# Kernel optimization log

Measured on AMD Instinct MI355X. Metric: run time of the kernel, lower is better.

The kernel has to match this reference:

```python
import jax, jax.numpy as jnp
import numpy as np

NUM_HEADS = 16

def setup_inputs() -> dict:
    key = jax.random.key(0)
    ks = jax.random.split(key, 5)
    B, L, H = 4, 1024, 1024
    s = 0.02
    return {
        'x': jax.random.normal(ks[0], (B, L, H), jnp.float32),
        'Wq': jax.random.normal(ks[1], (H, H), jnp.float32) * s,
        'Wkv_short': jax.random.normal(ks[2], (H, 2 * H), jnp.float32) * s,
        'Wkv_long': jax.random.normal(ks[3], (H, 2 * H), jnp.float32) * s,
        'Wo': jax.random.normal(ks[4], (H, H), jnp.float32) * s,
        'mix_weight': jnp.float32(0.5),
        'decay_factor': jnp.float32(0.95),
    }

def _heads(t, B, L, nh, hd):
    # [B, L, H] -> [B, nh, L, hd]
    return t.reshape(B, L, nh, hd).transpose(0, 2, 1, 3)

def _attention(q, k, v, bias):
    # q,k,v: [B, nh, L, hd]; bias: [L, L] or None
    hd = q.shape[-1]
    scores = jnp.einsum('bhqd,bhkd->bhqk', q, k) / jnp.sqrt(jnp.float32(hd))
    if bias is not None:
        scores = scores + bias[None, None]
    attn = jax.nn.softmax(scores, axis=-1)
    return jnp.einsum('bhqk,bhkd->bhqd', attn, v)

def reference(x, Wq, Wkv_short, Wkv_long, Wo, mix_weight, decay_factor):
    B, L, H = x.shape
    nh = NUM_HEADS
    hd = H // nh
    q = _heads(x @ Wq, B, L, nh, hd)
    kv_s = x @ Wkv_short
    k_s = _heads(kv_s[..., :H], B, L, nh, hd)
    v_s = _heads(kv_s[..., H:], B, L, nh, hd)
    pos = jnp.arange(L, dtype=jnp.float32)
    decay_bias = -jnp.abs(pos[None, :] - pos[:, None]) * (1.0 - decay_factor)
    out_short = _attention(q, k_s, v_s, decay_bias)
    kv_l = x @ Wkv_long
    k_l = _heads(kv_l[..., :H], B, L, nh, hd)
    v_l = _heads(kv_l[..., H:], B, L, nh, hd)
    out_long = _attention(q, k_l, v_l, None)
    alpha = jax.nn.sigmoid(mix_weight)
    out = alpha * out_short + (1.0 - alpha) * out_long
    out = out.transpose(0, 2, 1, 3).reshape(B, L, H)
    return out @ Wo
```

## Files before the change

### kernel.cpp

```cpp
#include <hip/hip_runtime.h>
#include <hip/hip_bf16.h>
#include <math.h>
#include <stdint.h>

typedef unsigned short u16;
typedef __attribute__((ext_vector_type(8))) short bf16x8;
typedef __attribute__((ext_vector_type(4))) float f32x4;
typedef __attribute__((ext_vector_type(4))) unsigned short u16x4;
typedef __attribute__((ext_vector_type(4))) unsigned int uint32x4;

#define MFMA_BF16(A, B, C) __builtin_amdgcn_mfma_f32_16x16x32_bf16((A), (B), (C), 0, 0, 0)

__device__ __forceinline__ void async16(const void* g, const void* l) {
    __builtin_amdgcn_global_load_lds(
        (const __attribute__((address_space(1))) unsigned int*)(uintptr_t)g,
        (__attribute__((address_space(3))) unsigned int*)(uintptr_t)l, 16, 0, 0);
}

__device__ __forceinline__ u16 f2bf(float f) {
    unsigned u = __float_as_uint(f);
    u += 0x7fffu + ((u >> 16) & 1u);
    return (u16)(u >> 16);
}

__device__ __forceinline__ unsigned pack2(float a, float b) {
    __hip_bfloat162 h = __float22bfloat162_rn(float2{a, b});
    return *reinterpret_cast<unsigned*>(&h);
}

__device__ __forceinline__ float bf2f(u16 v) {
    unsigned u = ((unsigned)v) << 16;
    return __uint_as_float(u);
}

__device__ __forceinline__ bf16x8 mk_frag(unsigned w0, unsigned w1,
                                          unsigned w2, unsigned w3) {
    uint32x4 u = {w0, w1, w2, w3};
    return __builtin_bit_cast(bf16x8, u);
}

__global__ __launch_bounds__(256) void cvt_x(const float* __restrict__ x,
                                             u16* __restrict__ xb) {
    int i = blockIdx.x * 256 + threadIdx.x;
    float4 v = ((const float4*)x)[i];
    u16x4 o = {f2bf(v.x), f2bf(v.y), f2bf(v.z), f2bf(v.w)};
    ((u16x4*)xb)[i] = o;
}

__global__ __launch_bounds__(256) void cvt_w_all(
    const float* __restrict__ Wq, const float* __restrict__ Wks,
    const float* __restrict__ Wkl, const float* __restrict__ Wo,
    u16* __restrict__ wqt, u16* __restrict__ wkst,
    u16* __restrict__ wklt, u16* __restrict__ wot)
{
    __shared__ float tile[32][33];
    int x = blockIdx.x;
    const float* W; u16* Wt; int N, nb;
    if (x < 32)       { W = Wq;  Wt = wqt;  N = 1024; nb = x * 32; }
    else if (x < 96)  { W = Wks; Wt = wkst; N = 2048; nb = (x - 32) * 32; }
    else if (x < 160) { W = Wkl; Wt = wklt; N = 2048; nb = (x - 96) * 32; }
    else              { W = Wo;  Wt = wot;  N = 1024; nb = (x - 160) * 32; }
    int kb = blockIdx.y * 32;
    int t = threadIdx.x;
    int r = t >> 3, c4 = (t & 7) * 4;
    float4 v = *(const float4*)&W[(size_t)(kb + r) * N + nb + c4];
    tile[r][c4] = v.x; tile[r][c4 + 1] = v.y;
    tile[r][c4 + 2] = v.z; tile[r][c4 + 3] = v.w;
    __syncthreads();
    u16x4 o = {f2bf(tile[c4 + 0][r]), f2bf(tile[c4 + 1][r]),
               f2bf(tile[c4 + 2][r]), f2bf(tile[c4 + 3][r])};
    *(u16x4*)&Wt[(size_t)(nb + r) * 1024 + kb + c4] = o;
}

__global__ __launch_bounds__(256) void gemm_proj(
    const u16* __restrict__ A, const u16* __restrict__ wq,
    const u16* __restrict__ wks, const u16* __restrict__ wkl,
    u16* __restrict__ qd, u16* __restrict__ ksd, u16* __restrict__ vsd,
    u16* __restrict__ kld, u16* __restrict__ vld)
{
    __shared__ u16 Alds[128][32];
    __shared__ u16 Blds[128][32];
    const int cx = blockIdx.x;
    const u16* Bt; u16* dK; u16* dV; int colBase; float osc = 1.0f;
    bool ktype;
    if (cx < 8)       { Bt = wq;  colBase = cx * 128;        dK = qd;  dV = nullptr;
                        osc = 0.18033688f; ktype = true; }
    else if (cx < 24) { Bt = wks; colBase = (cx - 8) * 128;  dK = ksd; dV = vsd;
                        ktype = (cx < 16); }
    else              { Bt = wkl; colBase = (cx - 24) * 128; dK = kld; dV = vld;
                        ktype = (cx < 32); }

    const int t = threadIdx.x;
    const int l = t & 63, w = t >> 6;
    const int wm = w & 1, wn = w >> 1;
    const int rowBase = blockIdx.y * 128;
    const int lc = l & 15, lr4 = l >> 4;

    f32x4 acc[4][4];
#pragma unroll
    for (int i = 0; i < 4; i++)
#pragma unroll
        for (int j = 0; j < 4; j++) acc[i][j] = (f32x4){0.f, 0.f, 0.f, 0.f};

    const int srow = w * 32 + (l >> 2);
    const int sc8  = (((l & 3) ^ ((l >> 2) & 3)) * 8);
    const u16* Ag = A  + (size_t)(rowBase + srow) * 1024 + sc8;
    const u16* Bg = Bt + (size_t)(colBase + srow) * 1024 + sc8;
    const int sw = (lc & 3);

    const u16 (*Lm)[32] = ktype ? Blds : Alds;
    const u16 (*Ln)[32] = ktype ? Alds : Blds;

    for (int kt = 0; kt < 32; ++kt) {
        __syncthreads();
        const int ko = kt * 32;
        async16(Ag + ko,         &Alds[w * 32][0]);
        async16(Ag + ko + 16384, &Alds[w * 32 + 16][0]);
        async16(Bg + ko,         &Blds[w * 32][0]);
        async16(Bg + ko + 16384, &Blds[w * 32 + 16][0]);
        __syncthreads();

        bf16x8 af[4], bf[4];
#pragma unroll
        for (int mt = 0; mt < 4; ++mt)
            af[mt] = *(const bf16x8*)&Lm[wm * 64 + mt * 16 + lc][(lr4 ^ sw) * 8];
#pragma unroll
        for (int nt = 0; nt < 4; ++nt)
            bf[nt] = *(const bf16x8*)&Ln[wn * 64 + nt * 16 + lc][(lr4 ^ sw) * 8];
#pragma unroll
        for (int mt = 0; mt < 4; ++mt)
#pragma unroll
            for (int nt = 0; nt < 4; ++nt)
                acc[mt][nt] = MFMA_BF16(af[mt], bf[nt], acc[mt][nt]);
    }

    if (ktype) {
#pragma unroll
        for (int mt = 0; mt < 4; ++mt)
#pragma unroll
            for (int nt = 0; nt < 4; ++nt) {
                int f   = colBase + wm * 64 + mt * 16 + lr4 * 4;
                int tok = rowBase + wn * 64 + nt * 16 + lc;
                int b = tok >> 10, tk = tok & 1023;
                int head = (f >> 6) & 15, d = f & 63;
                u16x4 pv = {f2bf(acc[mt][nt][0] * osc), f2bf(acc[mt][nt][1] * osc),
                            f2bf(acc[mt][nt][2] * osc), f2bf(acc[mt][nt][3] * osc)};
                *(u16x4*)&dK[((size_t)(b * 16 + head) * 1024 + tk) * 64 + d] = pv;
            }
    } else {
#pragma unroll
        for (int mt = 0; mt < 4; ++mt)
#pragma unroll
            for (int nt = 0; nt < 4; ++nt) {
                int gr0 = rowBase + wm * 64 + mt * 16 + lr4 * 4;
                int gc0 = colBase + wn * 64 + nt * 16;
                int head = gc0 >> 6;
                int b = gr0 >> 10, tok = gr0 & 1023;
                int tokp = (tok & ~31) | (((tok >> 2) & 3) << 3) |
                           (((tok >> 4) & 1) << 2);
                int d = (gc0 & 63) + lc;
                u16x4 pv = {f2bf(acc[mt][nt][0]), f2bf(acc[mt][nt][1]),
                            f2bf(acc[mt][nt][2]), f2bf(acc[mt][nt][3])};
                *(u16x4*)&dV[((size_t)(b * 16 + head - 16) * 64 + d) * 1024 +
                             tokp] = pv;
            }
    }
}

__global__ __launch_bounds__(256) void gemm_out(
    const u16* __restrict__ Aattn, const u16* __restrict__ Bwot,
    float* __restrict__ dst)
{
    __shared__ u16 Alds[64][32];
    __shared__ u16 Blds[128][32];
    const int t = threadIdx.x;
    const int l = t & 63, w = t >> 6;
    const int wm = w & 1, wn = w >> 1;
    const int rowBase = blockIdx.y * 64;
    const int colBase = blockIdx.x * 128;
    const int lc = l & 15, lr4 = l >> 4;

    f32x4 acc[4][2];
#pragma unroll
    for (int i = 0; i < 4; i++)
#pragma unroll
        for (int j = 0; j < 2; j++) acc[i][j] = (f32x4){0.f, 0.f, 0.f, 0.f};

    const int sl  = l >> 2;
    const int sc8 = (((l & 3) ^ (sl & 3)) * 8);
    const u16* Ag = Aattn + (size_t)(rowBase + w * 16 + sl) * 1024 + sc8;
    const u16* Bg = Bwot  + (size_t)(colBase + w * 32 + sl) * 1024 + sc8;
    const int sw = (lc & 3);

    for (int kt = 0; kt < 32; ++kt) {
        __syncthreads();
        const int ko = kt * 32;
        async16(Ag + ko,         &Alds[w * 16][0]);
        async16(Bg + ko,         &Blds[w * 32][0]);
        async16(Bg + ko + 16384, &Blds[w * 32 + 16][0]);
        __syncthreads();

        bf16x8 af[4], bf[2];
#pragma unroll
        for (int mt = 0; mt < 4; ++mt)
            af[mt] = *(const bf16x8*)&Blds[wm * 64 + mt * 16 + lc][(lr4 ^ sw) * 8];
#pragma unroll
        for (int nt = 0; nt < 2; ++nt)
            bf[nt] = *(const bf16x8*)&Alds[wn * 32 + nt * 16 + lc][(lr4 ^ sw) * 8];
#pragma unroll
        for (int mt = 0; mt < 4; ++mt)
#pragma unroll
            for (int nt = 0; nt < 2; ++nt)
                acc[mt][nt] = MFMA_BF16(af[mt], bf[nt], acc[mt][nt]);
    }

#pragma unroll
    for (int mt = 0; mt < 4; ++mt)
#pragma unroll
        for (int nt = 0; nt < 2; ++nt) {
            int f   = colBase + wm * 64 + mt * 16 + lr4 * 4;
            int tok = rowBase + wn * 32 + nt * 16 + lc;
            float4 v = {acc[mt][nt][0], acc[mt][nt][1],
                        acc[mt][nt][2], acc[mt][nt][3]};
            *(float4*)&dst[(size_t)tok * 1024 + f] = v;
        }
}

__global__ __launch_bounds__(256, 4) void attn_mfma(
    const u16* __restrict__ Q, const u16* __restrict__ Ksb,
    const u16* __restrict__ Vsb, const u16* __restrict__ Klb,
    const u16* __restrict__ Vlb, const float* __restrict__ decayf,
    u16* __restrict__ Os, u16* __restrict__ Ol)
{
    __shared__ __align__(16) u16 Kt[2][2][64][32];
    __shared__ __align__(16) u16 Vt[2][2][64][32];

    const int t = threadIdx.x;
    const int l = t & 63, w = t >> 6;
    const int lc = l & 15, lr4 = l >> 4;
    const int h = blockIdx.x, qt = blockIdx.y;
    const int b = blockIdx.z >> 1, branch = blockIdx.z & 1;
    const size_t bh = (size_t)(b * 16 + h);
    const int qbase = qt * 128;
    const u16* Qg = Q + bh * (1024 * 64);
    const u16* Kg = (branch ? Klb : Ksb) + bh * (1024 * 64);
    const u16* Vg = (branch ? Vlb : Vsb) + bh * (64 * 1024);
    u16* outp = branch ? Ol : Os;

    const int sl = l >> 2;
    const int sc = (((l & 3) ^ ((l >> 3) & 3)) * 8);
    const int swr = (lc >> 1) & 3;

    int ktLo = 0, ktHi = 16;
    if (branch == 0) {
        ktLo = qt * 2 - 7; if (ktLo < 0) ktLo = 0;
        ktHi = qt * 2 + 9; if (ktHi > 16) ktHi = 16;
    }

    bf16x8 aQ[2][2];
#pragma unroll
    for (int qg = 0; qg < 2; ++qg)
#pragma unroll
        for (int kh = 0; kh < 2; ++kh)
            aQ[qg][kh] = *(const bf16x8*)&Qg[
                (size_t)(qbase + w * 32 + qg * 16 + lc) * 64 + kh * 32 + lr4 * 8];

    auto stage = [&](int kt, int buf) {
#pragma unroll
        for (int i = 0; i < 4; i++) {
            int id = w * 4 + i;
            int kh = (id >> 2) & 1, ch = id & 3;
            if (id < 8)
                async16(Kg + (size_t)(kt * 64 + ch * 16 + sl) * 64 + kh * 32 + sc,
                        &Kt[buf][kh][ch * 16][0]);
            else
                async16(Vg + (size_t)(ch * 16 + sl) * 1024 + kt * 64 + kh * 32 + sc,
                        &Vt[buf][kh][ch * 16][0]);
        }
    };

    stage(ktLo, 0);
    __syncthreads();

    const float C2 = (1.0f - decayf[0]) * 1.44269504f;
    const float qf = (float)(qbase + w * 32 + lc);

    f32x4 sumv[2] = {(f32x4){0.f, 0.f, 0.f, 0.f}, (f32x4){0.f, 0.f, 0.f, 0.f}};
    f32x4 o[2][4];
#pragma unroll
    for (int qg = 0; qg < 2; ++qg)
#pragma unroll
        for (int dt = 0; dt < 4; ++dt) o[qg][dt] = (f32x4){0.f, 0.f, 0.f, 0.f};

    for (int kt = ktLo, it = 0; kt < ktHi; ++kt, ++it) {
        const int cur = it & 1;
        if (kt + 1 < ktHi) stage(kt + 1, cur ^ 1);

        bf16x8 ak[4][2];
#pragma unroll
        for (int nt = 0; nt < 4; ++nt) {
            ak[nt][0] = *(const bf16x8*)&Kt[cur][0][nt * 16 + lc][(lr4 ^ swr) * 8];
            ak[nt][1] = *(const bf16x8*)&Kt[cur][1][nt * 16 + lc][(lr4 ^ swr) * 8];
        }

        unsigned pw[2][8];
#pragma unroll
        for (int qg = 0; qg < 2; ++qg) {
            const float d0 = qf + (float)(qg * 16 - kt * 64 - lr4 * 4);
            f32x4 s[4];
#pragma unroll
            for (int nt = 0; nt < 4; ++nt) {
                if (branch == 0) {
                    float dd = d0 - (float)(nt * 16);
                    s[nt] = (f32x4){-fabsf(dd) * C2,
                                    -fabsf(dd - 1.0f) * C2,
                                    -fabsf(dd - 2.0f) * C2,
                                    -fabsf(dd - 3.0f) * C2};
                } else {
                    s[nt] = (f32x4){0.f, 0.f, 0.f, 0.f};
                }
                s[nt] = MFMA_BF16(ak[nt][0], aQ[qg][0], s[nt]);
                s[nt] = MFMA_BF16(ak[nt][1], aQ[qg][1], s[nt]);
            }
#pragma unroll
            for (int nt = 0; nt < 4; ++nt) {
                float p0 = __builtin_amdgcn_exp2f(s[nt][0]);
                float p1 = __builtin_amdgcn_exp2f(s[nt][1]);
                float p2 = __builtin_amdgcn_exp2f(s[nt][2]);
                float p3 = __builtin_amdgcn_exp2f(s[nt][3]);
                sumv[qg][0] += p0; sumv[qg][1] += p1;
                sumv[qg][2] += p2; sumv[qg][3] += p3;
                pw[qg][nt * 2]     = pack2(p0, p1);
                pw[qg][nt * 2 + 1] = pack2(p2, p3);
            }
        }

#pragma unroll
        for (int dt = 0; dt < 4; ++dt) {
            bf16x8 v0 = *(const bf16x8*)&Vt[cur][0][dt * 16 + lc][(lr4 ^ swr) * 8];
            bf16x8 v1 = *(const bf16x8*)&Vt[cur][1][dt * 16 + lc][(lr4 ^ swr) * 8];
#pragma unroll
            for (int qg = 0; qg < 2; ++qg) {
                bf16x8 pb0 = mk_frag(pw[qg][0], pw[qg][1], pw[qg][2], pw[qg][3]);
                bf16x8 pb1 = mk_frag(pw[qg][4], pw[qg][5], pw[qg][6], pw[qg][7]);
                o[qg][dt] = MFMA_BF16(v0, pb0, o[qg][dt]);
                o[qg][dt] = MFMA_BF16(v1, pb1, o[qg][dt]);
            }
        }

        __syncthreads();
    }

#pragma unroll
    for (int qg = 0; qg < 2; ++qg) {
        float s = (sumv[qg][0] + sumv[qg][1]) + (sumv[qg][2] + sumv[qg][3]);
        s += __shfl_xor(s, 16);
        s += __shfl_xor(s, 32);
        float inv = 1.0f / s;
        int qrow = qbase + w * 32 + qg * 16 + lc;
        u16* op = outp + ((size_t)(b * 1024) + qrow) * 1024 + h * 64;
#pragma unroll
        for (int dt = 0; dt < 4; ++dt) {
            uint2 w2 = {pack2(o[qg][dt][0] * inv, o[qg][dt][1] * inv),
                        pack2(o[qg][dt][2] * inv, o[qg][dt][3] * inv)};
            *(uint2*)&op[dt * 16 + lr4 * 4] = w2;
        }
    }
}

__global__ __launch_bounds__(256) void mix_kernel(
    const u16* __restrict__ Os, const u16* __restrict__ Ol,
    const float* __restrict__ mixw, u16* __restrict__ dst)
{
    const float a = 1.0f / (1.0f + __expf(-mixw[0]));
    int i = blockIdx.x * 256 + threadIdx.x;
    uint4 s = ((const uint4*)Os)[i];
    uint4 l = ((const uint4*)Ol)[i];
    unsigned su[4] = {s.x, s.y, s.z, s.w};
    unsigned lu[4] = {l.x, l.y, l.z, l.w};
    unsigned ou[4];
#pragma unroll
    for (int k = 0; k < 4; ++k) {
        float s0 = bf2f((u16)su[k]), s1 = bf2f((u16)(su[k] >> 16));
        float l0 = bf2f((u16)lu[k]), l1 = bf2f((u16)(lu[k] >> 16));
        ou[k] = pack2(l0 + a * (s0 - l0), l1 + a * (s1 - l1));
    }
    ((uint4*)dst)[i] = make_uint4(ou[0], ou[1], ou[2], ou[3]);
}

extern "C" void kernel_launch(void* const* d_in, const int* in_sizes, int n_in,
                              void* d_out, int out_size, void* d_ws, size_t ws_size,
                              hipStream_t stream) {
    const float* x      = (const float*)d_in[0];
    const float* Wq     = (const float*)d_in[1];
    const float* Wkvs   = (const float*)d_in[2];
    const float* Wkvl   = (const float*)d_in[3];
    const float* Wo     = (const float*)d_in[4];
    const float* mixw   = (const float*)d_in[5];
    const float* decayf = (const float*)d_in[6];

    const size_t M1 = 1024 * 1024;
    u16* ws    = (u16*)d_ws;
    u16* xb    = ws;
    u16* wqt   = xb + 4 * M1;
    u16* wkvst = wqt + 1 * M1;
    u16* wkvlt = wkvst + 2 * M1;
    u16* wot   = wkvlt + 2 * M1;
    u16* qb    = wot + 1 * M1;
    u16* ksb   = qb + 4 * M1;
    u16* vsb   = ksb + 4 * M1;
    u16* klb   = vsb + 4 * M1;
    u16* vlb   = klb + 4 * M1;
    u16* attnb = vlb + 4 * M1;
    u16* osb   = xb;
    u16* olb   = wqt;

    cvt_x<<<4096, 256, 0, stream>>>(x, xb);
    cvt_w_all<<<dim3(192, 32), 256, 0, stream>>>(Wq, Wkvs, Wkvl, Wo,
                                                 wqt, wkvst, wkvlt, wot);
    gemm_proj<<<dim3(40, 32), 256, 0, stream>>>(xb, wqt, wkvst, wkvlt,
                                                qb, ksb, vsb, klb, vlb);
    attn_mfma<<<dim3(16, 8, 8), 256, 0, stream>>>(qb, ksb, vsb, klb, vlb,
                                                  decayf, osb, olb);
    mix_kernel<<<2048, 256, 0, stream>>>(osb, olb, mixw, attnb);
    gemm_out<<<dim3(8, 64), 256, 0, stream>>>(attnb, wot, (float*)d_out);
}
```

Baseline: 232.1 us.

## Double-buffer projection GEMM LDS and widen tiles to 128x256

The projection GEMM now uses 128x256 output tiles (a 4x8 MFMA accumulator grid per wave) and double-buffers the async global-to-LDS loads, so the next K slice is fetched while the current one is multiplied. This drops one barrier per iteration and halves the block count, aiming to hide load latency and raise arithmetic intensity. The cost is more registers and LDS per block, which lowers occupancy and parallelism (a 640-block grid, with launch bounds requesting 2 blocks per CU). V-output head indexing is adjusted to the new local column base.

Result: slower. 238.3 us (+2.7%).

```diff
diff --git a/kernel.cpp b/kernel.cpp
--- a/kernel.cpp
+++ b/kernel.cpp
@@ -72,75 +72,97 @@
     *(u16x4*)&Wt[(size_t)(nb + r) * 1024 + kb + c4] = o;
 }
 
-__global__ __launch_bounds__(256) void gemm_proj(
+__global__ __launch_bounds__(256, 2) void gemm_proj(
     const u16* __restrict__ A, const u16* __restrict__ wq,
     const u16* __restrict__ wks, const u16* __restrict__ wkl,
     u16* __restrict__ qd, u16* __restrict__ ksd, u16* __restrict__ vsd,
     u16* __restrict__ kld, u16* __restrict__ vld)
 {
-    __shared__ u16 Alds[128][32];
-    __shared__ u16 Blds[128][32];
+    __shared__ u16 Alds[2][128][32];
+    __shared__ u16 Blds[2][256][32];
     const int cx = blockIdx.x;
-    const u16* Bt; u16* dK; u16* dV; int colBase; float osc = 1.0f;
+    const u16* Bt; u16* dK; u16* dV; int colMat, colLoc; float osc = 1.0f;
     bool ktype;
-    if (cx < 8)       { Bt = wq;  colBase = cx * 128;        dK = qd;  dV = nullptr;
-                        osc = 0.18033688f; ktype = true; }
-    else if (cx < 24) { Bt = wks; colBase = (cx - 8) * 128;  dK = ksd; dV = vsd;
-                        ktype = (cx < 16); }
-    else              { Bt = wkl; colBase = (cx - 24) * 128; dK = kld; dV = vld;
-                        ktype = (cx < 32); }
+    if (cx < 4) {
+        Bt = wq; ktype = true; colLoc = cx * 256; colMat = colLoc;
+        dK = qd; dV = nullptr; osc = 0.18033688f;
+    } else if (cx < 12) {
+        Bt = wks; ktype = (cx < 8);
+        if (ktype) { colLoc = (cx - 4) * 256; colMat = colLoc; }
+        else       { colLoc = (cx - 8) * 256; colMat = 1024 + colLoc; }
+        dK = ksd; dV = vsd;
+    } else {
+        Bt = wkl; ktype = (cx < 16);
+        if (ktype) { colLoc = (cx - 12) * 256; colMat = colLoc; }
+        else       { colLoc = (cx - 16) * 256; colMat = 1024 + colLoc; }
+        dK = kld; dV = vld;
+    }
 
     const int t = threadIdx.x;
     const int l = t & 63, w = t >> 6;
-    const int wm = w & 1, wn = w >> 1;
     const int rowBase = blockIdx.y * 128;
     const int lc = l & 15, lr4 = l >> 4;
 
-    f32x4 acc[4][4];
+    f32x4 acc[4][8];
 #pragma unroll
     for (int i = 0; i < 4; i++)
 #pragma unroll
-        for (int j = 0; j < 4; j++) acc[i][j] = (f32x4){0.f, 0.f, 0.f, 0.f};
-
-    const int srow = w * 32 + (l >> 2);
-    const int sc8  = (((l & 3) ^ ((l >> 2) & 3)) * 8);
-    const u16* Ag = A  + (size_t)(rowBase + srow) * 1024 + sc8;
-    const u16* Bg = Bt + (size_t)(colBase + srow) * 1024 + sc8;
+        for (int j = 0; j < 8; j++) acc[i][j] = (f32x4){0.f, 0.f, 0.f, 0.f};
+
+    const int sl  = l >> 2;
+    const int sc8 = (((l & 3) ^ (sl & 3)) * 8);
+    const u16* Ag = A  + (size_t)(rowBase + w * 32 + sl) * 1024 + sc8;
+    const u16* Bg = Bt + (size_t)(colMat  + w * 64 + sl) * 1024 + sc8;
     const int sw = (lc & 3);
 
-    const u16 (*Lm)[32] = ktype ? Blds : Alds;
-    const u16 (*Ln)[32] = ktype ? Alds : Blds;
+    auto stage = [&](int kt, int buf) {
+        const int ko = kt * 32;
+        async16(Ag + ko,             &Alds[buf][w * 32][0]);
+        async16(Ag + ko + 16 * 1024, &Alds[buf][w * 32 + 16][0]);
+        async16(Bg + ko,             &Blds[buf][w * 64][0]);
+        async16(Bg + ko + 16 * 1024, &Blds[buf][w * 64 + 16][0]);
+        async16(Bg + ko + 32 * 1024, &Blds[buf][w * 64 + 32][0]);
+        async16(Bg + ko + 48 * 1024, &Blds[buf][w * 64 + 48][0]);
+    };
+
+    const int mOff = ktype ? w * 64 : (w & 1) * 64;
+    const int nOff = ktype ? 0      : (w >> 1) * 128;
+
+    stage(0, 0);
+    __syncthreads();
 
     for (int kt = 0; kt < 32; ++kt) {
+        const int cur = kt & 1;
+        if (kt + 1 < 32) stage(kt + 1, cur ^ 1);
+
+        const u16 (*Ab)[32] = Alds[cur];
+        const u16 (*Bb)[32] = Blds[cur];
+        const u16 (*Lm)[32] = ktype ? Bb : Ab;
+        const u16 (*Ln)[32] = ktype ? Ab : Bb;
+
+        bf16x8 af[4], bf[8];
+#pragma unroll
+        for (int mt = 0; mt < 4; ++mt)
+            af[mt] = *(const bf16x8*)&Lm[mOff + mt * 16 + lc][(lr4 ^ sw) * 8];
+#pragma unroll
+        for (int nt = 0; nt < 8; ++nt)
+            bf[nt] = *(const bf16x8*)&Ln[nOff + nt * 16 + lc][(lr4 ^ sw) * 8];
+#pragma unroll
+        for (int mt = 0; mt < 4; ++mt)
+#pragma unroll
+            for (int nt = 0; nt < 8; ++nt)
+                acc[mt][nt] = MFMA_BF16(af[mt], bf[nt], acc[mt][nt]);
+
         __syncthreads();
-        const int ko = kt * 32;
-        async16(Ag + ko,         &Alds[w * 32][0]);
-        async16(Ag + ko + 16384, &Alds[w * 32 + 16][0]);
-        async16(Bg + ko,         &Blds[w * 32][0]);
-        async16(Bg + ko + 16384, &Blds[w * 32 + 16][0]);
-        __syncthreads();
-
-        bf16x8 af[4], bf[4];
-#pragma unroll
-        for (int mt = 0; mt < 4; ++mt)
-            af[mt] = *(const bf16x8*)&Lm[wm * 64 + mt * 16 + lc][(lr4 ^ sw) * 8];
-#pragma unroll
-        for (int nt = 0; nt < 4; ++nt)
-            bf[nt] = *(const bf16x8*)&Ln[wn * 64 + nt * 16 + lc][(lr4 ^ sw) * 8];
-#pragma unroll
-        for (int mt = 0; mt < 4; ++mt)
-#pragma unroll
-            for (int nt = 0; nt < 4; ++nt)
-                acc[mt][nt] = MFMA_BF16(af[mt], bf[nt], acc[mt][nt]);
     }
 
     if (ktype) {
 #pragma unroll
         for (int mt = 0; mt < 4; ++mt)
 #pragma unroll
-            for (int nt = 0; nt < 4; ++nt) {
-                int f   = colBase + wm * 64 + mt * 16 + lr4 * 4;
-                int tok = rowBase + wn * 64 + nt * 16 + lc;
+            for (int nt = 0; nt < 8; ++nt) {
+                int f   = colLoc + w * 64 + mt * 16 + lr4 * 4;
+                int tok = rowBase + nt * 16 + lc;
                 int b = tok >> 10, tk = tok & 1023;
                 int head = (f >> 6) & 15, d = f & 63;
                 u16x4 pv = {f2bf(acc[mt][nt][0] * osc), f2bf(acc[mt][nt][1] * osc),
@@ -151,9 +173,9 @@
 #pragma unroll
         for (int mt = 0; mt < 4; ++mt)
 #pragma unroll
-            for (int nt = 0; nt < 4; ++nt) {
-                int gr0 = rowBase + wm * 64 + mt * 16 + lr4 * 4;
-                int gc0 = colBase + wn * 64 + nt * 16;
+            for (int nt = 0; nt < 8; ++nt) {
+                int gr0 = rowBase + (w & 1) * 64 + mt * 16 + lr4 * 4;
+                int gc0 = colLoc + (w >> 1) * 128 + nt * 16;
                 int head = gc0 >> 6;
                 int b = gr0 >> 10, tok = gr0 & 1023;
                 int tokp = (tok & ~31) | (((tok >> 2) & 3) << 3) |
@@ -161,7 +183,7 @@
                 int d = (gc0 & 63) + lc;
                 u16x4 pv = {f2bf(acc[mt][nt][0]), f2bf(acc[mt][nt][1]),
                             f2bf(acc[mt][nt][2]), f2bf(acc[mt][nt][3])};
-                *(u16x4*)&dV[((size_t)(b * 16 + head - 16) * 64 + d) * 1024 +
+                *(u16x4*)&dV[((size_t)(b * 16 + head) * 64 + d) * 1024 +
                              tokp] = pv;
             }
     }
@@ -418,7 +440,7 @@
     cvt_x<<<4096, 256, 0, stream>>>(x, xb);
     cvt_w_all<<<dim3(192, 32), 256, 0, stream>>>(Wq, Wkvs, Wkvl, Wo,
                                                  wqt, wkvst, wkvlt, wot);
-    gemm_proj<<<dim3(40, 32), 256, 0, stream>>>(xb, wqt, wkvst, wkvlt,
+    gemm_proj<<<dim3(20, 32), 256, 0, stream>>>(xb, wqt, wkvst, wkvlt,
                                                 qb, ksb, vsb, klb, vlb);
     attn_mfma<<<dim3(16, 8, 8), 256, 0, stream>>>(qb, ksb, vsb, klb, vlb,
                                                   decayf, osb, olb);
```

## Double-buffer projection GEMM LDS tiles and swizzle workgroup order for XCD locality

Applied to the files above, without the earlier changes.

The projection GEMM now stages the next K-tile into a second LDS buffer while computing on the current one, dropping one of the two barriers per iteration. It also remaps workgroup IDs so that workgroups landing on the same XCD (wg & 7) process contiguous tiles, and applies a similar remap to the output GEMM, to improve L2 reuse. Launch bounds hint 3 waves-per-EU occupancy. The cost is doubled LDS use for gemm_proj. Correctness relies on global_load_lds completing before the trailing barrier; no explicit vmcnt wait is visible.

Result: no change. 236.0 us (+1.7%).

```diff
diff --git a/kernel.cpp b/kernel.cpp
--- a/kernel.cpp
+++ b/kernel.cpp
@@ -72,15 +72,20 @@
     *(u16x4*)&Wt[(size_t)(nb + r) * 1024 + kb + c4] = o;
 }
 
-__global__ __launch_bounds__(256) void gemm_proj(
+__global__ __launch_bounds__(256, 3) void gemm_proj(
     const u16* __restrict__ A, const u16* __restrict__ wq,
     const u16* __restrict__ wks, const u16* __restrict__ wkl,
     u16* __restrict__ qd, u16* __restrict__ ksd, u16* __restrict__ vsd,
     u16* __restrict__ kld, u16* __restrict__ vld)
 {
-    __shared__ u16 Alds[128][32];
-    __shared__ u16 Blds[128][32];
-    const int cx = blockIdx.x;
+    __shared__ u16 Alds[2][128][32];
+    __shared__ u16 Blds[2][128][32];
+
+    const int wg  = blockIdx.y * 40 + blockIdx.x;
+    const int swz = (wg & 7) * 160 + (wg >> 3);
+    const int cx  = swz % 40;
+    const int rowBase = (swz / 40) * 128;
+
     const u16* Bt; u16* dK; u16* dV; int colBase; float osc = 1.0f;
     bool ktype;
     if (cx < 8)       { Bt = wq;  colBase = cx * 128;        dK = qd;  dV = nullptr;
@@ -93,7 +98,6 @@
     const int t = threadIdx.x;
     const int l = t & 63, w = t >> 6;
     const int wm = w & 1, wn = w >> 1;
-    const int rowBase = blockIdx.y * 128;
     const int lc = l & 15, lr4 = l >> 4;
 
     f32x4 acc[4][4];
@@ -108,17 +112,23 @@
     const u16* Bg = Bt + (size_t)(colBase + srow) * 1024 + sc8;
     const int sw = (lc & 3);
 
-    const u16 (*Lm)[32] = ktype ? Blds : Alds;
-    const u16 (*Ln)[32] = ktype ? Alds : Blds;
+    auto stage = [&](int kt, int buf) {
+        const int ko = kt * 32;
+        async16(Ag + ko,         &Alds[buf][w * 32][0]);
+        async16(Ag + ko + 16384, &Alds[buf][w * 32 + 16][0]);
+        async16(Bg + ko,         &Blds[buf][w * 32][0]);
+        async16(Bg + ko + 16384, &Blds[buf][w * 32 + 16][0]);
+    };
+
+    stage(0, 0);
+    __syncthreads();
 
     for (int kt = 0; kt < 32; ++kt) {
-        __syncthreads();
-        const int ko = kt * 32;
-        async16(Ag + ko,         &Alds[w * 32][0]);
-        async16(Ag + ko + 16384, &Alds[w * 32 + 16][0]);
-        async16(Bg + ko,         &Blds[w * 32][0]);
-        async16(Bg + ko + 16384, &Blds[w * 32 + 16][0]);
-        __syncthreads();
+        const int cur = kt & 1;
+        if (kt + 1 < 32) stage(kt + 1, cur ^ 1);
+
+        const u16 (*Lm)[32] = ktype ? Blds[cur] : Alds[cur];
+        const u16 (*Ln)[32] = ktype ? Alds[cur] : Blds[cur];
 
         bf16x8 af[4], bf[4];
 #pragma unroll
@@ -132,6 +142,8 @@
 #pragma unroll
             for (int nt = 0; nt < 4; ++nt)
                 acc[mt][nt] = MFMA_BF16(af[mt], bf[nt], acc[mt][nt]);
+
+        __syncthreads();
     }
 
     if (ktype) {
@@ -176,8 +188,12 @@
     const int t = threadIdx.x;
     const int l = t & 63, w = t >> 6;
     const int wm = w & 1, wn = w >> 1;
-    const int rowBase = blockIdx.y * 64;
-    const int colBase = blockIdx.x * 128;
+
+    const int wg  = blockIdx.y * 8 + blockIdx.x;
+    const int swz = (wg & 7) * 64 + (wg >> 3);
+    const int rowBase = (swz >> 3) * 64;
+    const int colBase = (swz & 7) * 128;
+
     const int lc = l & 15, lr4 = l >> 4;
 
     f32x4 acc[4][2];
```
